# Kernel tuning notes

Measured on AMD Instinct MI355X. Metric: run time of the kernel, lower is better.

## Reference

```python
import jax, jax.numpy as jnp
import numpy as np

B, E, K, P, C = 4096, 8, 4, 96, 32  # samples, experts, top_k, pred_len, channels
EPS = 2.220446049250313e-16  # np.finfo(float).eps, as in the torch code


def setup_inputs() -> dict:
    key = jax.random.key(0)
    k1, k2 = jax.random.split(key)
    # Build sparse top-k gates exactly as the upstream router would: topk + softmax, scattered dense.
    logits = jax.random.normal(k1, (B, E), dtype=jnp.float32)
    top_vals, top_idx = jax.lax.top_k(logits, K)
    top_w = jax.nn.softmax(top_vals, axis=-1)
    gates = jnp.zeros((B, E), dtype=jnp.float32).at[jnp.arange(B)[:, None], top_idx].set(top_w)
    # Dispatch indices: torch does nonzero(gates).sort(0) -> entries grouped by expert.
    mask = np.asarray(gates) > 0
    b_idx, e_idx = np.nonzero(mask)                  # row-major: sorted by batch then expert
    order = np.argsort(e_idx, kind='stable')         # group by expert (== torch.cat over per-expert xs)
    batch_index = jnp.asarray(b_idx[order], dtype=jnp.int64)
    expert_index = jnp.asarray(e_idx[order], dtype=jnp.int64)
    # Stitched expert outputs [N=B*K, P, C]; modest scale since forward applies exp().
    x = jax.random.normal(k2, (B * K, P, C), dtype=jnp.float32) * 0.5
    return {"x": x, "gates": gates, "batch_index": batch_index, "expert_index": expert_index}


def reference(x, gates, batch_index, expert_index):
    # _nonzero_gates = gather(gates[_batch_index], 1, _expert_index)
    nz_gates = gates[batch_index, expert_index]                      # [N]
    # stitched = cat(xs).exp() scaled per-sample by its gate weight
    stitched = jnp.exp(x) * nz_gates[:, None, None]                  # [N, P, C]
    # combined = zeros(B,P,C).index_add(0, batch_index, stitched)
    combined = jnp.zeros((gates.shape[0], x.shape[1], x.shape[2]), dtype=x.dtype)
    combined = combined.at[batch_index].add(stitched)
    # combined[combined == 0] = eps; log
    combined = jnp.where(combined == 0, jnp.asarray(EPS, combined.dtype), combined)
    return jnp.log(combined)
```

## Files before the change

### kernel.cpp

```cpp
#include <hip/hip_runtime.h>

#define BATCH 4096
#define NEXP 8
#define TOPK 4
#define PC 3072
#define EPSV 2.220446049250313e-16f

__global__ void build_inv_kernel(const int* __restrict__ batch_index,
                                 const int* __restrict__ expert_index,
                                 const float* __restrict__ gates,
                                 int* __restrict__ cnt,
                                 int* __restrict__ inv,
                                 float* __restrict__ gval,
                                 int N) {
    int n = blockIdx.x * blockDim.x + threadIdx.x;
    if (n >= N) return;
    int b = batch_index[n];
    int e = expert_index[n];
    int slot = atomicAdd(&cnt[b], 1);
    if (slot < TOPK) {
        inv[b * TOPK + slot]  = n;
        gval[b * TOPK + slot] = gates[b * NEXP + e];
    }
}

__global__ __launch_bounds__(256) void combine_kernel(
        const float* __restrict__ x,
        const int* __restrict__ inv,
        const float* __restrict__ gval,
        float* __restrict__ out) {
    const int b = blockIdx.x;
    const int t = threadIdx.x;

    int   n0 = inv[b * TOPK + 0], n1 = inv[b * TOPK + 1],
          n2 = inv[b * TOPK + 2], n3 = inv[b * TOPK + 3];
    float g0 = gval[b * TOPK + 0], g1 = gval[b * TOPK + 1],
          g2 = gval[b * TOPK + 2], g3 = gval[b * TOPK + 3];

    #define CSWAP(na, ga, nb, gb) { if (na > nb) { int tn = na; na = nb; nb = tn; float tg = ga; ga = gb; gb = tg; } }
    CSWAP(n0, g0, n1, g1); CSWAP(n2, g2, n3, g3);
    CSWAP(n0, g0, n2, g2); CSWAP(n1, g1, n3, g3);
    CSWAP(n1, g1, n2, g2);
    #undef CSWAP

    const float4* x0 = (const float4*)(x + (long long)n0 * PC);
    const float4* x1 = (const float4*)(x + (long long)n1 * PC);
    const float4* x2 = (const float4*)(x + (long long)n2 * PC);
    const float4* x3 = (const float4*)(x + (long long)n3 * PC);
    float4* o = (float4*)(out + (long long)b * PC);

    #pragma unroll
    for (int j = 0; j < 3; ++j) {
        const int f = t + j * 256;
        float4 a0 = x0[f];
        float4 a1 = x1[f];
        float4 a2 = x2[f];
        float4 a3 = x3[f];
        float4 r;
        r.x = g0 * __expf(a0.x) + g1 * __expf(a1.x) + g2 * __expf(a2.x) + g3 * __expf(a3.x);
        r.y = g0 * __expf(a0.y) + g1 * __expf(a1.y) + g2 * __expf(a2.y) + g3 * __expf(a3.y);
        r.z = g0 * __expf(a0.z) + g1 * __expf(a1.z) + g2 * __expf(a2.z) + g3 * __expf(a3.z);
        r.w = g0 * __expf(a0.w) + g1 * __expf(a1.w) + g2 * __expf(a2.w) + g3 * __expf(a3.w);
        r.x = __logf(r.x == 0.0f ? EPSV : r.x);
        r.y = __logf(r.y == 0.0f ? EPSV : r.y);
        r.z = __logf(r.z == 0.0f ? EPSV : r.z);
        r.w = __logf(r.w == 0.0f ? EPSV : r.w);
        o[f] = r;
    }
}

extern "C" void kernel_launch(void* const* d_in, const int* in_sizes, int n_in,
                              void* d_out, int out_size, void* d_ws, size_t ws_size,
                              hipStream_t stream) {
    const float* x           = (const float*)d_in[0];
    const float* gates       = (const float*)d_in[1];
    const int*   batch_index = (const int*)d_in[2];
    const int*   expert_index= (const int*)d_in[3];
    float* out = (float*)d_out;
    const int N = in_sizes[2];

    int*   cnt  = (int*)d_ws;
    int*   inv  = cnt + BATCH;
    float* gval = (float*)(inv + BATCH * TOPK);
    const size_t zero_bytes = (size_t)BATCH * sizeof(int)
                            + (size_t)BATCH * TOPK * sizeof(int)
                            + (size_t)BATCH * TOPK * sizeof(float);

    hipMemsetAsync(d_ws, 0, zero_bytes, stream);

    build_inv_kernel<<<(N + 255) / 256, 256, 0, stream>>>(
        batch_index, expert_index, gates, cnt, inv, gval, N);

    combine_kernel<<<BATCH, 256, 0, stream>>>(x, inv, gval, out);
}
```

Before: 49.78 us.

## Compute dispatch slots deterministically and drop memset; batch nontemporal loads in combine

The inverse-index build now derives each entry's slot from the count of nonzero gates with lower expert index in the same row. This removes the atomic counter and the workspace memset, saving a launch. Because entries within a row are grouped by expert, slot order follows n order, so the sorting network in the combine kernel is dropped. The combine kernel issues all twelve vector loads up front as nontemporal loads and writes with nontemporal stores, aiming for more memory-level parallelism and less cache pollution. The new slot logic relies on exactly TOPK positive gates per row; it no longer guards against overflow.

```diff
diff --git a/kernel.cpp b/kernel.cpp
--- a/kernel.cpp
+++ b/kernel.cpp
@@ -6,22 +6,26 @@
 #define PC 3072
 #define EPSV 2.220446049250313e-16f
 
-__global__ void build_inv_kernel(const int* __restrict__ batch_index,
-                                 const int* __restrict__ expert_index,
-                                 const float* __restrict__ gates,
-                                 int* __restrict__ cnt,
-                                 int* __restrict__ inv,
-                                 float* __restrict__ gval,
-                                 int N) {
+typedef float f32x4 __attribute__((ext_vector_type(4)));
+
+__global__ __launch_bounds__(256) void build_inv_kernel(
+        const int* __restrict__ batch_index,
+        const int* __restrict__ expert_index,
+        const float* __restrict__ gates,
+        int* __restrict__ inv,
+        float* __restrict__ gval,
+        int N) {
     int n = blockIdx.x * blockDim.x + threadIdx.x;
     if (n >= N) return;
     int b = batch_index[n];
     int e = expert_index[n];
-    int slot = atomicAdd(&cnt[b], 1);
-    if (slot < TOPK) {
-        inv[b * TOPK + slot]  = n;
-        gval[b * TOPK + slot] = gates[b * NEXP + e];
-    }
+    const float* grow = gates + b * NEXP;
+    int slot = 0;
+    #pragma unroll
+    for (int q = 0; q < NEXP - 1; ++q)
+        slot += (q < e && grow[q] > 0.0f) ? 1 : 0;
+    inv[b * TOPK + slot]  = n;
+    gval[b * TOPK + slot] = grow[e];
 }
 
 __global__ __launch_bounds__(256) void combine_kernel(
@@ -32,64 +36,54 @@
     const int b = blockIdx.x;
     const int t = threadIdx.x;
 
-    int   n0 = inv[b * TOPK + 0], n1 = inv[b * TOPK + 1],
-          n2 = inv[b * TOPK + 2], n3 = inv[b * TOPK + 3];
-    float g0 = gval[b * TOPK + 0], g1 = gval[b * TOPK + 1],
-          g2 = gval[b * TOPK + 2], g3 = gval[b * TOPK + 3];
+    const int   n0 = inv[b * TOPK + 0], n1 = inv[b * TOPK + 1],
+                n2 = inv[b * TOPK + 2], n3 = inv[b * TOPK + 3];
+    const float g0 = gval[b * TOPK + 0], g1 = gval[b * TOPK + 1],
+                g2 = gval[b * TOPK + 2], g3 = gval[b * TOPK + 3];
 
-    #define CSWAP(na, ga, nb, gb) { if (na > nb) { int tn = na; na = nb; nb = tn; float tg = ga; ga = gb; gb = tg; } }
-    CSWAP(n0, g0, n1, g1); CSWAP(n2, g2, n3, g3);
-    CSWAP(n0, g0, n2, g2); CSWAP(n1, g1, n3, g3);
-    CSWAP(n1, g1, n2, g2);
-    #undef CSWAP
+    const f32x4* x0 = (const f32x4*)(x + (size_t)n0 * PC) + t;
+    const f32x4* x1 = (const f32x4*)(x + (size_t)n1 * PC) + t;
+    const f32x4* x2 = (const f32x4*)(x + (size_t)n2 * PC) + t;
+    const f32x4* x3 = (const f32x4*)(x + (size_t)n3 * PC) + t;
+    f32x4* o = (f32x4*)(out + (size_t)b * PC) + t;
 
-    const float4* x0 = (const float4*)(x + (long long)n0 * PC);
-    const float4* x1 = (const float4*)(x + (long long)n1 * PC);
-    const float4* x2 = (const float4*)(x + (long long)n2 * PC);
-    const float4* x3 = (const float4*)(x + (long long)n3 * PC);
-    float4* o = (float4*)(out + (long long)b * PC);
+    f32x4 a0[3], a1[3], a2[3], a3[3];
+    #pragma unroll
+    for (int j = 0; j < 3; ++j) {
+        a0[j] = __builtin_nontemporal_load(x0 + j * 256);
+        a1[j] = __builtin_nontemporal_load(x1 + j * 256);
+        a2[j] = __builtin_nontemporal_load(x2 + j * 256);
+        a3[j] = __builtin_nontemporal_load(x3 + j * 256);
+    }
 
     #pragma unroll
     for (int j = 0; j < 3; ++j) {
-        const int f = t + j * 256;
-        float4 a0 = x0[f];
-        float4 a1 = x1[f];
-        float4 a2 = x2[f];
-        float4 a3 = x3[f];
-        float4 r;
-        r.x = g0 * __expf(a0.x) + g1 * __expf(a1.x) + g2 * __expf(a2.x) + g3 * __expf(a3.x);
-        r.y = g0 * __expf(a0.y) + g1 * __expf(a1.y) + g2 * __expf(a2.y) + g3 * __expf(a3.y);
-        r.z = g0 * __expf(a0.z) + g1 * __expf(a1.z) + g2 * __expf(a2.z) + g3 * __expf(a3.z);
-        r.w = g0 * __expf(a0.w) + g1 * __expf(a1.w) + g2 * __expf(a2.w) + g3 * __expf(a3.w);
-        r.x = __logf(r.x == 0.0f ? EPSV : r.x);
-        r.y = __logf(r.y == 0.0f ? EPSV : r.y);
-        r.z = __logf(r.z == 0.0f ? EPSV : r.z);
-        r.w = __logf(r.w == 0.0f ? EPSV : r.w);
-        o[f] = r;
+        f32x4 r;
+        #pragma unroll
+        for (int c = 0; c < 4; ++c) {
+            float s = g0 * __expf(a0[j][c]) + g1 * __expf(a1[j][c])
+                    + g2 * __expf(a2[j][c]) + g3 * __expf(a3[j][c]);
+            r[c] = __logf(s == 0.0f ? EPSV : s);
+        }
+        __builtin_nontemporal_store(r, o + j * 256);
     }
 }
 
 extern "C" void kernel_launch(void* const* d_in, const int* in_sizes, int n_in,
                               void* d_out, int out_size, void* d_ws, size_t ws_size,
                               hipStream_t stream) {
-    const float* x           = (const float*)d_in[0];
-    const float* gates       = (const float*)d_in[1];
-    const int*   batch_index = (const int*)d_in[2];
-    const int*   expert_index= (const int*)d_in[3];
+    const float* x            = (const float*)d_in[0];
+    const float* gates        = (const float*)d_in[1];
+    const int*   batch_index  = (const int*)d_in[2];
+    const int*   expert_index = (const int*)d_in[3];
     float* out = (float*)d_out;
     const int N = in_sizes[2];
 
-    int*   cnt  = (int*)d_ws;
-    int*   inv  = cnt + BATCH;
+    int*   inv  = (int*)d_ws;
     float* gval = (float*)(inv + BATCH * TOPK);
-    const size_t zero_bytes = (size_t)BATCH * sizeof(int)
-                            + (size_t)BATCH * TOPK * sizeof(int)
-                            + (size_t)BATCH * TOPK * sizeof(float);
-
-    hipMemsetAsync(d_ws, 0, zero_bytes, stream);
 
     build_inv_kernel<<<(N + 255) / 256, 256, 0, stream>>>(
-        batch_index, expert_index, gates, cnt, inv, gval, N);
+        batch_index, expert_index, gates, inv, gval, N);
 
     combine_kernel<<<BATCH, 256, 0, stream>>>(x, inv, gval, out);
 }
```

Measured after the change: 48.67 us. 1.02x faster.
